# Kernel optimization log

Hardware: AMD Instinct MI355X
Metric: run time of the kernel (lower is better)

## Reference

```python
import jax, jax.numpy as jnp
import numpy as np

B_, T_, DIN, H, DZ, DX = 64, 256, 128, 256, 8, 8


def setup_inputs() -> dict:
    key = jax.random.key(0)
    ks = jax.random.split(key, 13)
    p = lambda k, sh: jax.random.normal(k, sh, dtype=jnp.float32) * 0.05
    return {
        "y": jax.random.normal(ks[0], (B_, T_, DIN), dtype=jnp.float32),
        "W_ih": p(ks[1], (3 * H, DIN)), "W_hh": p(ks[2], (3 * H, H)),
        "b_ih": p(ks[3], (3 * H,)), "b_hh": p(ks[4], (3 * H,)),
        "W_mz": p(ks[5], (DZ, H)), "b_mz": p(ks[6], (DZ,)),
        "W_mx": p(ks[7], (DX, H)), "b_mx": p(ks[8], (DX,)),
        "W_pz": p(ks[9], (2 * DZ, H)), "b_pz": p(ks[10], (2 * DZ,)),
        "W_cx": p(ks[11], (DX * DX, H)), "b_cx": p(ks[12], (DX * DX,)),
    }


def _gru(y, W_ih, W_hh, b_ih, b_hh):
    # torch nn.GRU (single layer, unidirectional, batch_first)
    B, T, _ = y.shape
    Hh = W_hh.shape[1]
    x_proj = jnp.einsum('btd,gd->btg', y, W_ih) + b_ih  # [B,T,3H]

    def step(h, xp):
        hp = h @ W_hh.T + b_hh
        xr, xz, xn = jnp.split(xp, 3, axis=-1)
        hr, hz, hn = jnp.split(hp, 3, axis=-1)
        r = jax.nn.sigmoid(xr + hr)
        z = jax.nn.sigmoid(xz + hz)
        n = jnp.tanh(xn + r * hn)
        h_new = (1.0 - z) * n + z * h
        return h_new, h_new

    h0 = jnp.zeros((B, Hh), dtype=y.dtype)
    _, hs = jax.lax.scan(step, h0, jnp.swapaxes(x_proj, 0, 1))
    return jnp.swapaxes(hs, 0, 1)  # [B,T,H]


def _forward(y, W_ih, W_hh, b_ih, b_hh, W_mz, b_mz, W_mx, b_mx, W_pz, b_pz, W_cx, b_cx):
    enc = _gru(y, W_ih, W_hh, b_ih, b_hh)                       # [B,T,H]
    mean_z = enc @ W_mz.T + b_mz                                 # [B,T,DZ]
    mean_x = enc @ W_mx.T + b_mx                                 # [B,T,DX]
    bd_z = enc @ W_pz.T + b_pz                                   # [B,T,2*DZ]  (apply_softplus=False)

    # banded cov: per latent dim, upper-bidiagonal cholesky factor [B,T,T]
    diag = jnp.moveaxis(jax.nn.softplus(bd_z[..., :DZ]), -1, 0)  # [DZ,B,T]
    off = jnp.moveaxis(bd_z[:, :-1, DZ:], -1, 0)                 # [DZ,B,T-1]
    B, T = diag.shape[1], diag.shape[2]
    idx = jnp.arange(T)
    chol_z = (jnp.zeros((DZ, B, T, T), dtype=y.dtype)
              .at[:, :, idx, idx].set(diag)
              .at[:, :, idx[:-1], idx[1:]].set(off))             # [DZ,B,T,T]

    # anchor first two x-dims at t=0 (in-place mutation in torch)
    mean_x = mean_x.at[:, :, :2].add(-mean_x[:, 0:1, :2])
    mean_x_flat = mean_x.reshape(B * T, DX)

    cov_x = enc @ W_cx.T + b_cx                                  # [B,T,DX*DX]
    cov_x_flat = cov_x.reshape(B * T, DX, DX)
    return mean_z, chol_z, mean_x_flat, cov_x_flat


def reference(y, W_ih, W_hh, b_ih, b_hh, W_mz, b_mz, W_mx, b_mx, W_pz, b_pz, W_cx, b_cx):
    return _forward(y, W_ih, W_hh, b_ih, b_hh, W_mz, b_mz, W_mx, b_mx, W_pz, b_pz, W_cx, b_cx)
```

## Files before the change

kernel.cpp:

```cpp
#include <hip/hip_runtime.h>
#include <cstdint>
#include <cstddef>

#define B_   64
#define T_   256
#define DIN_ 128
#define H_   256
#define G3_  768

__device__ __forceinline__ unsigned short f2h(float f) {
  _Float16 h = (_Float16)f;
  return __builtin_bit_cast(unsigned short, h);
}

__device__ __forceinline__ void dot2f(float& acc, unsigned a, unsigned b) {
  asm("v_dot2_f32_f16 %0, %1, %2, %0" : "+v"(acc) : "v"(a), "v"(b));
}

__global__ __launch_bounds__(256) void prep_kernel(
    const float* __restrict__ W_ih, const float* __restrict__ W_hh,
    const float* __restrict__ W_mz, const float* __restrict__ W_mx,
    const float* __restrict__ W_pz, const float* __restrict__ W_cx,
    float* __restrict__ WT_ih, float* __restrict__ WheadT,
    unsigned* __restrict__ Wreg) {
  int i = blockIdx.x * 256 + threadIdx.x;
  if (i < 98304) {
    int k = i / 768, g = i % 768;
    WT_ih[i] = W_ih[g * 128 + k];
  } else if (i < 98304 + 24576) {
    int j = i - 98304;
    int c = j >> 8, k = j & 255;
    float v;
    if (c < 8)       v = W_mz[c * 256 + k];
    else if (c < 16) v = W_mx[(c - 8) * 256 + k];
    else if (c < 32) v = W_pz[(c - 16) * 256 + k];
    else             v = W_cx[(c - 32) * 256 + k];
    WheadT[j] = v;
  } else {
    int m = i - 122880;
    int c = m & 3, n = m >> 2;
    int t = n & 511, j4 = n >> 9;
    int j = 4 * j4 + c;
    int a = j >> 5, qp = j & 31;
    int o = a * 128 + (t & 127);
    int k0 = ((t >> 7) << 6) + 2 * qp;
    unsigned short lo = f2h(W_hh[o * 256 + k0]);
    unsigned short hi = f2h(W_hh[o * 256 + k0 + 1]);
    Wreg[m] = ((unsigned)hi << 16) | (unsigned)lo;
  }
}

__global__ __launch_bounds__(256) void xproj_kernel(
    const float* __restrict__ y, const float* __restrict__ WT_ih,
    const float* __restrict__ b_ih, float* __restrict__ xp) {
  __shared__ float ylds[32][132];
  int tid = threadIdx.x;
  int row0 = blockIdx.x * 32;
  const float4* y4 = (const float4*)(y + (size_t)row0 * DIN_);
#pragma unroll
  for (int i = 0; i < 4; ++i) {
    int idx = i * 256 + tid;
    float4 v = y4[idx];
    int r = idx >> 5, c4 = (idx & 31) * 4;
    ylds[r][c4 + 0] = v.x; ylds[r][c4 + 1] = v.y;
    ylds[r][c4 + 2] = v.z; ylds[r][c4 + 3] = v.w;
  }
  __syncthreads();
  int tx = tid & 15, ty = tid >> 4;
  for (int c = 0; c < 6; ++c) {
    int col0 = c * 128 + tx * 8;
    float acc[2][8];
#pragma unroll
    for (int a = 0; a < 2; ++a)
#pragma unroll
      for (int b = 0; b < 8; ++b) acc[a][b] = 0.f;
#pragma unroll 4
    for (int k = 0; k < 128; ++k) {
      float4 w0 = *(const float4*)&WT_ih[k * 768 + col0];
      float4 w1 = *(const float4*)&WT_ih[k * 768 + col0 + 4];
      float a0 = ylds[ty * 2 + 0][k], a1 = ylds[ty * 2 + 1][k];
      acc[0][0] += a0 * w0.x; acc[0][1] += a0 * w0.y; acc[0][2] += a0 * w0.z; acc[0][3] += a0 * w0.w;
      acc[0][4] += a0 * w1.x; acc[0][5] += a0 * w1.y; acc[0][6] += a0 * w1.z; acc[0][7] += a0 * w1.w;
      acc[1][0] += a1 * w0.x; acc[1][1] += a1 * w0.y; acc[1][2] += a1 * w0.z; acc[1][3] += a1 * w0.w;
      acc[1][4] += a1 * w1.x; acc[1][5] += a1 * w1.y; acc[1][6] += a1 * w1.z; acc[1][7] += a1 * w1.w;
    }
    float4 b0 = *(const float4*)&b_ih[col0];
    float4 b1 = *(const float4*)&b_ih[col0 + 4];
#pragma unroll
    for (int a = 0; a < 2; ++a) {
      int row = row0 + ty * 2 + a;
      float4 o0, o1;
      o0.x = acc[a][0] + b0.x; o0.y = acc[a][1] + b0.y; o0.z = acc[a][2] + b0.z; o0.w = acc[a][3] + b0.w;
      o1.x = acc[a][4] + b1.x; o1.y = acc[a][5] + b1.y; o1.z = acc[a][6] + b1.z; o1.w = acc[a][7] + b1.w;
      *(float4*)&xp[(size_t)row * G3_ + col0] = o0;
      *(float4*)&xp[(size_t)row * G3_ + col0 + 4] = o1;
    }
  }
}

__global__ __launch_bounds__(512) __attribute__((amdgpu_waves_per_eu(2, 2)))
void gru_kernel(
    const float* __restrict__ xp, const unsigned* Wreg,
    const float* __restrict__ b_hh, float* enc) {
  int tid = threadIdx.x;
  int ks = tid >> 7;
  int og = tid & 127;
  int b = blockIdx.x;
  __shared__ alignas(16) unsigned short hsb[256];
  __shared__ alignas(16) float part[3104];
  unsigned w[192];
  const uint4* W4 = (const uint4*)Wreg;
#pragma unroll
  for (int j4 = 0; j4 < 48; ++j4) {
    uint4 q = W4[j4 * 512 + tid];
    w[4 * j4 + 0] = q.x; w[4 * j4 + 1] = q.y;
    w[4 * j4 + 2] = q.z; w[4 * j4 + 3] = q.w;
  }
  const float* xpb = xp + (size_t)b * (T_ * G3_);
  float* encb = enc + (size_t)b * (T_ * H_);
  float bhr = 0.f, bhz = 0.f, bhn = 0.f, hold = 0.f;
  float xr0 = 0.f, xz0 = 0.f, xn0 = 0.f, xr1 = 0.f, xz1 = 0.f, xn1 = 0.f;
  if (tid < 256) {
    bhr = b_hh[tid]; bhz = b_hh[256 + tid]; bhn = b_hh[512 + tid];
    xr0 = xpb[tid];        xz0 = xpb[256 + tid];        xn0 = xpb[512 + tid];
    xr1 = xpb[768 + tid];  xz1 = xpb[1024 + tid];       xn1 = xpb[1280 + tid];
    hsb[tid] = 0;
  }
  __syncthreads();
  for (int t = 0; t < T_; ++t) {
    asm volatile("" ::: "memory");
    float xr2 = 0.f, xz2 = 0.f, xn2 = 0.f;
    if (tid < 256) {
      int base = (t + 2) * G3_ + tid;
      xr2 = xpb[base]; xz2 = xpb[base + 256]; xn2 = xpb[base + 512];
    }
    float p0 = 0.f, p1 = 0.f, p2 = 0.f, p3 = 0.f, p4 = 0.f, p5 = 0.f;
    const uint4* hs = ((const uint4*)hsb) + (ks << 3);
#pragma unroll
    for (int r = 0; r < 8; ++r) {
      uint4 hq = hs[r];
      dot2f(p0, hq.x, w[(r << 2) + 0]);
      dot2f(p0, hq.y, w[(r << 2) + 1]);
      dot2f(p0, hq.z, w[(r << 2) + 2]);
      dot2f(p0, hq.w, w[(r << 2) + 3]);
      dot2f(p1, hq.x, w[32 + (r << 2) + 0]);
      dot2f(p1, hq.y, w[32 + (r << 2) + 1]);
      dot2f(p1, hq.z, w[32 + (r << 2) + 2]);
      dot2f(p1, hq.w, w[32 + (r << 2) + 3]);
      dot2f(p2, hq.x, w[64 + (r << 2) + 0]);
      dot2f(p2, hq.y, w[64 + (r << 2) + 1]);
      dot2f(p2, hq.z, w[64 + (r << 2) + 2]);
      dot2f(p2, hq.w, w[64 + (r << 2) + 3]);
      dot2f(p3, hq.x, w[96 + (r << 2) + 0]);
      dot2f(p3, hq.y, w[96 + (r << 2) + 1]);
      dot2f(p3, hq.z, w[96 + (r << 2) + 2]);
      dot2f(p3, hq.w, w[96 + (r << 2) + 3]);
      dot2f(p4, hq.x, w[128 + (r << 2) + 0]);
      dot2f(p4, hq.y, w[128 + (r << 2) + 1]);
      dot2f(p4, hq.z, w[128 + (r << 2) + 2]);
      dot2f(p4, hq.w, w[128 + (r << 2) + 3]);
      dot2f(p5, hq.x, w[160 + (r << 2) + 0]);
      dot2f(p5, hq.y, w[160 + (r << 2) + 1]);
      dot2f(p5, hq.z, w[160 + (r << 2) + 2]);
      dot2f(p5, hq.w, w[160 + (r << 2) + 3]);
    }
    int pb = ks * 776 + og;
    part[pb]       = p0;  part[pb + 128] = p1;
    part[pb + 256] = p2;  part[pb + 384] = p3;
    part[pb + 512] = p4;  part[pb + 640] = p5;
    __syncthreads();
    if (tid < 256) {
      int u = tid;
      float prer = bhr + ((part[u] + part[776 + u]) +
                          (part[1552 + u] + part[2328 + u]));
      float prez = bhz + ((part[256 + u] + part[1032 + u]) +
                          (part[1808 + u] + part[2584 + u]));
      float pren = bhn + ((part[512 + u] + part[1288 + u]) +
                          (part[2064 + u] + part[2840 + u]));
      float r_ = 1.f / (1.f + __expf(-(xr0 + prer)));
      float z_ = 1.f / (1.f + __expf(-(xz0 + prez)));
      float a = xn0 + r_ * pren;
      a = fminf(15.f, fmaxf(-15.f, a));
      float e = __expf(2.f * a);
      float n = (e - 1.f) / (e + 1.f);
      float hnew = (1.f - z_) * n + z_ * hold;
      hold = hnew;
      encb[t * H_ + u] = hnew;
      hsb[u] = f2h(hnew);
      xr0 = xr1; xz0 = xz1; xn0 = xn1;
      xr1 = xr2; xz1 = xz2; xn1 = xn2;
    }
    __syncthreads();
  }
}

__global__ void anchor_kernel(const float* __restrict__ enc,
                              const float* __restrict__ W_mx,
                              const float* __restrict__ b_mx,
                              float* __restrict__ anchor) {
  int tid = threadIdx.x;
  if (tid < 128) {
    int b = tid >> 1, d = tid & 1;
    const float* e = enc + (size_t)b * T_ * H_;
    float acc = b_mx[d];
    for (int k = 0; k < 256; ++k) acc += e[k] * W_mx[d * 256 + k];
    anchor[b * 2 + d] = acc;
  }
}

__global__ __launch_bounds__(384) void heads_kernel(
    const float* __restrict__ enc, const float* __restrict__ WheadT,
    const float* __restrict__ b_mz, const float* __restrict__ b_mx,
    const float* __restrict__ b_pz, const float* __restrict__ b_cx,
    const float* __restrict__ anchor,
    float* __restrict__ out_meanz, float* __restrict__ out_meanx,
    float* __restrict__ out_covx, float* __restrict__ stage) {
  __shared__ float el[32 * 256];
  int tid = threadIdx.x;
  int row0 = blockIdx.x * 32;
  const float4* e4 = (const float4*)(enc + (size_t)row0 * 256);
  float4* el4 = (float4*)el;
#pragma unroll
  for (int i = 0; i < 6; ++i) {
    int idx = i * 384 + tid;
    if (idx < 2048) el4[idx] = e4[idx];
  }
  __syncthreads();
  int rg = tid / 96, c = tid - rg * 96;
  const float4* Wc = (const float4*)(WheadT + c * 256);
  float acc[8];
#pragma unroll
  for (int r = 0; r < 8; ++r) acc[r] = 0.f;
  for (int k4 = 0; k4 < 64; ++k4) {
    float4 w4 = Wc[k4];
#pragma unroll
    for (int r = 0; r < 8; ++r) {
      float4 ev = el4[(rg * 8 + r) * 64 + k4];
      acc[r] += w4.x * ev.x; acc[r] += w4.y * ev.y;
      acc[r] += w4.z * ev.z; acc[r] += w4.w * ev.w;
    }
  }
#pragma unroll
  for (int r = 0; r < 8; ++r) {
    int row = row0 + rg * 8 + r;
    int bb = row >> 8;
    float a_ = acc[r];
    if (c < 8) {
      out_meanz[(size_t)row * 8 + c] = a_ + b_mz[c];
    } else if (c < 16) {
      int d = c - 8;
      float v = a_ + b_mx[d];
      if (d < 2) v -= anchor[bb * 2 + d];
      out_meanx[(size_t)row * 8 + d] = v;
    } else if (c < 32) {
      int d = c - 16;
      float v = a_ + b_pz[d];
      if (d < 8)
        v = (v > 0.f) ? (v + log1pf(__expf(-v))) : log1pf(__expf(v));
      stage[(size_t)row * 16 + d] = v;
    } else {
      int d = c - 32;
      out_covx[(size_t)row * 64 + d] = a_ + b_cx[d];
    }
  }
}

__global__ __launch_bounds__(256) void chol_kernel(
    const float* __restrict__ stage, float4* __restrict__ chol) {
  int i = blockIdx.x * 256 + threadIdx.x;
  int stride = gridDim.x * 256;
  for (; i < 8388608; i += stride) {
    int d = i >> 20;
    int bt = (i >> 6) & 16383;
    int t = bt & 255;
    int lane = i & 63;
    float vd = 0.f, vo = 0.f;
    if ((t >> 2) == lane)        vd = stage[bt * 16 + d];
    if (((t + 1) >> 2) == lane)  vo = stage[bt * 16 + 8 + d];
    int te = t & 3, oe = (t + 1) & 3;
    float4 v;
    v.x = (te == 0 ? vd : 0.f) + (oe == 0 ? vo : 0.f);
    v.y = (te == 1 ? vd : 0.f) + (oe == 1 ? vo : 0.f);
    v.z = (te == 2 ? vd : 0.f) + (oe == 2 ? vo : 0.f);
    v.w = (te == 3 ? vd : 0.f) + (oe == 3 ? vo : 0.f);
    chol[i] = v;
  }
}

extern "C" void kernel_launch(void* const* d_in, const int* in_sizes, int n_in,
                              void* d_out, int out_size, void* d_ws, size_t ws_size,
                              hipStream_t stream) {
  const float* y    = (const float*)d_in[0];
  const float* W_ih = (const float*)d_in[1];
  const float* W_hh = (const float*)d_in[2];
  const float* b_ih = (const float*)d_in[3];
  const float* b_hh = (const float*)d_in[4];
  const float* W_mz = (const float*)d_in[5];
  const float* b_mz = (const float*)d_in[6];
  const float* W_mx = (const float*)d_in[7];
  const float* b_mx = (const float*)d_in[8];
  const float* W_pz = (const float*)d_in[9];
  const float* b_pz = (const float*)d_in[10];
  const float* W_cx = (const float*)d_in[11];
  const float* b_cx = (const float*)d_in[12];

  float* out    = (float*)d_out;
  float* mean_z = out;
  float* chol   = out + 131072;
  float* mean_x = out + 33685504;
  float* cov_x  = out + 33816576;

  float* ws      = (float*)d_ws;
  float* WT_ih   = ws;
  float* WheadT  = ws + 98304;
  unsigned* Wreg = (unsigned*)(ws + 122880);
  float* anchor  = ws + 221184;
  float* stage   = ws + 221312;

  float* xp  = chol;
  float* enc = chol + 12582912;

  prep_kernel<<<864, 256, 0, stream>>>(W_ih, W_hh, W_mz, W_mx, W_pz, W_cx,
                                       WT_ih, WheadT, Wreg);
  xproj_kernel<<<512, 256, 0, stream>>>(y, WT_ih, b_ih, xp);
  gru_kernel<<<64, 512, 0, stream>>>(xp, Wreg, b_hh, enc);
  anchor_kernel<<<1, 128, 0, stream>>>(enc, W_mx, b_mx, anchor);
  heads_kernel<<<512, 384, 0, stream>>>(enc, WheadT, b_mz, b_mx, b_pz, b_cx,
                                        anchor, mean_z, mean_x, cov_x, stage);
  chol_kernel<<<8192, 256, 0, stream>>>(stage, (float4*)chol);
}
```

Measured before the change: 620.3 us.

## Fuse input projection into GRU kernel with flag-based streaming and split chol zeroing

Merges the x-projection GEMM and the GRU recurrence into one launch. 64 recurrence blocks spin on per-chunk release/acquire flags while 256 extra blocks compute xp in 64-row chunks, so the recurrence can start before the whole projection finishes. It also parallelises the anchor reduction across 128 blocks. The zero-fill of the upper half of chol_z (latent dims 4-7) moves into extra heads_kernel blocks, and chol_fin only writes the diagonals for those dims, which shortens the tail pass. The cost is a forward-progress dependency: the spin-waiting blocks need the producer blocks to be scheduled alongside them, plus extra flag traffic.

```diff
diff --git a/kernel.cpp b/kernel.cpp
--- a/kernel.cpp
+++ b/kernel.cpp
@@ -17,13 +17,18 @@
   asm("v_dot2_f32_f16 %0, %1, %2, %0" : "+v"(acc) : "v"(a), "v"(b));
 }
 
+__device__ __forceinline__ int load_acq(const int* p) {
+  return __hip_atomic_load(p, __ATOMIC_ACQUIRE, __HIP_MEMORY_SCOPE_AGENT);
+}
+
 __global__ __launch_bounds__(256) void prep_kernel(
     const float* __restrict__ W_ih, const float* __restrict__ W_hh,
     const float* __restrict__ W_mz, const float* __restrict__ W_mx,
     const float* __restrict__ W_pz, const float* __restrict__ W_cx,
     float* __restrict__ WT_ih, float* __restrict__ WheadT,
-    unsigned* __restrict__ Wreg) {
+    unsigned* __restrict__ Wreg, int* __restrict__ done) {
   int i = blockIdx.x * 256 + threadIdx.x;
+  if (i < 512) done[i] = 0;
   if (i < 98304) {
     int k = i / 768, g = i % 768;
     WT_ih[i] = W_ih[g * 128 + k];
@@ -50,64 +55,73 @@
   }
 }
 
-__global__ __launch_bounds__(256) void xproj_kernel(
+__global__ __launch_bounds__(512) __attribute__((amdgpu_waves_per_eu(2, 2)))
+void fused_kernel(
     const float* __restrict__ y, const float* __restrict__ WT_ih,
-    const float* __restrict__ b_ih, float* __restrict__ xp) {
-  __shared__ float ylds[32][132];
+    const float* __restrict__ b_ih, float* xp,
+    const unsigned* Wreg, const float* __restrict__ b_hh,
+    float* enc, int* done) {
+  __shared__ alignas(16) unsigned char smem[34816];
   int tid = threadIdx.x;
-  int row0 = blockIdx.x * 32;
-  const float4* y4 = (const float4*)(y + (size_t)row0 * DIN_);
-#pragma unroll
-  for (int i = 0; i < 4; ++i) {
-    int idx = i * 256 + tid;
-    float4 v = y4[idx];
-    int r = idx >> 5, c4 = (idx & 31) * 4;
-    ylds[r][c4 + 0] = v.x; ylds[r][c4 + 1] = v.y;
-    ylds[r][c4 + 2] = v.z; ylds[r][c4 + 3] = v.w;
-  }
-  __syncthreads();
-  int tx = tid & 15, ty = tid >> 4;
-  for (int c = 0; c < 6; ++c) {
-    int col0 = c * 128 + tx * 8;
-    float acc[2][8];
-#pragma unroll
-    for (int a = 0; a < 2; ++a)
-#pragma unroll
-      for (int b = 0; b < 8; ++b) acc[a][b] = 0.f;
+
+  if (blockIdx.x >= 64) {
+    int j = blockIdx.x - 64;
+    int row0 = j * 64;
+    float* ylds = (float*)smem;
+    const float4* y4 = (const float4*)(y + (size_t)row0 * DIN_);
+#pragma unroll
+    for (int i = 0; i < 4; ++i) {
+      int idx = i * 512 + tid;
+      float4 v = y4[idx];
+      int r = idx >> 5, c4 = (idx & 31) * 4;
+      ylds[r * 132 + c4 + 0] = v.x; ylds[r * 132 + c4 + 1] = v.y;
+      ylds[r * 132 + c4 + 2] = v.z; ylds[r * 132 + c4 + 3] = v.w;
+    }
+    __syncthreads();
+    int tx = tid & 15, ty = tid >> 4;
+    for (int c = 0; c < 6; ++c) {
+      int col0 = c * 128 + tx * 8;
+      float acc[2][8];
+#pragma unroll
+      for (int a = 0; a < 2; ++a)
+#pragma unroll
+        for (int b2 = 0; b2 < 8; ++b2) acc[a][b2] = 0.f;
 #pragma unroll 4
-    for (int k = 0; k < 128; ++k) {
-      float4 w0 = *(const float4*)&WT_ih[k * 768 + col0];
-      float4 w1 = *(const float4*)&WT_ih[k * 768 + col0 + 4];
-      float a0 = ylds[ty * 2 + 0][k], a1 = ylds[ty * 2 + 1][k];
-      acc[0][0] += a0 * w0.x; acc[0][1] += a0 * w0.y; acc[0][2] += a0 * w0.z; acc[0][3] += a0 * w0.w;
-      acc[0][4] += a0 * w1.x; acc[0][5] += a0 * w1.y; acc[0][6] += a0 * w1.z; acc[0][7] += a0 * w1.w;
-      acc[1][0] += a1 * w0.x; acc[1][1] += a1 * w0.y; acc[1][2] += a1 * w0.z; acc[1][3] += a1 * w0.w;
-      acc[1][4] += a1 * w1.x; acc[1][5] += a1 * w1.y; acc[1][6] += a1 * w1.z; acc[1][7] += a1 * w1.w;
-    }
-    float4 b0 = *(const float4*)&b_ih[col0];
-    float4 b1 = *(const float4*)&b_ih[col0 + 4];
-#pragma unroll
-    for (int a = 0; a < 2; ++a) {
-      int row = row0 + ty * 2 + a;
-      float4 o0, o1;
-      o0.x = acc[a][0] + b0.x; o0.y = acc[a][1] + b0.y; o0.z = acc[a][2] + b0.z; o0.w = acc[a][3] + b0.w;
-      o1.x = acc[a][4] + b1.x; o1.y = acc[a][5] + b1.y; o1.z = acc[a][6] + b1.z; o1.w = acc[a][7] + b1.w;
-      *(float4*)&xp[(size_t)row * G3_ + col0] = o0;
-      *(float4*)&xp[(size_t)row * G3_ + col0 + 4] = o1;
-    }
-  }
-}
-
-__global__ __launch_bounds__(512) __attribute__((amdgpu_waves_per_eu(2, 2)))
-void gru_kernel(
-    const float* __restrict__ xp, const unsigned* Wreg,
-    const float* __restrict__ b_hh, float* enc) {
-  int tid = threadIdx.x;
+      for (int k = 0; k < 128; ++k) {
+        float4 w0 = *(const float4*)&WT_ih[k * 768 + col0];
+        float4 w1 = *(const float4*)&WT_ih[k * 768 + col0 + 4];
+        float a0 = ylds[(ty * 2 + 0) * 132 + k];
+        float a1 = ylds[(ty * 2 + 1) * 132 + k];
+        acc[0][0] += a0 * w0.x; acc[0][1] += a0 * w0.y; acc[0][2] += a0 * w0.z; acc[0][3] += a0 * w0.w;
+        acc[0][4] += a0 * w1.x; acc[0][5] += a0 * w1.y; acc[0][6] += a0 * w1.z; acc[0][7] += a0 * w1.w;
+        acc[1][0] += a1 * w0.x; acc[1][1] += a1 * w0.y; acc[1][2] += a1 * w0.z; acc[1][3] += a1 * w0.w;
+        acc[1][4] += a1 * w1.x; acc[1][5] += a1 * w1.y; acc[1][6] += a1 * w1.z; acc[1][7] += a1 * w1.w;
+      }
+      float4 b0 = *(const float4*)&b_ih[col0];
+      float4 b1 = *(const float4*)&b_ih[col0 + 4];
+#pragma unroll
+      for (int a = 0; a < 2; ++a) {
+        int row = row0 + ty * 2 + a;
+        float4 o0, o1;
+        o0.x = acc[a][0] + b0.x; o0.y = acc[a][1] + b0.y; o0.z = acc[a][2] + b0.z; o0.w = acc[a][3] + b0.w;
+        o1.x = acc[a][4] + b1.x; o1.y = acc[a][5] + b1.y; o1.z = acc[a][6] + b1.z; o1.w = acc[a][7] + b1.w;
+        *(float4*)&xp[(size_t)row * G3_ + col0] = o0;
+        *(float4*)&xp[(size_t)row * G3_ + col0 + 4] = o1;
+      }
+    }
+    __syncthreads();
+    if (tid == 0) {
+      __threadfence();
+      __hip_atomic_store(&done[j], 1, __ATOMIC_RELEASE, __HIP_MEMORY_SCOPE_AGENT);
+    }
+    return;
+  }
+
   int ks = tid >> 7;
   int og = tid & 127;
   int b = blockIdx.x;
-  __shared__ alignas(16) unsigned short hsb[256];
-  __shared__ alignas(16) float part[3104];
+  unsigned short* hsb = (unsigned short*)smem;
+  float* part = (float*)(smem + 512);
   unsigned w[192];
   const uint4* W4 = (const uint4*)Wreg;
 #pragma unroll
@@ -118,6 +132,8 @@
   }
   const float* xpb = xp + (size_t)b * (T_ * G3_);
   float* encb = enc + (size_t)b * (T_ * H_);
+  if (tid == 0) { while (load_acq(&done[4 * b]) == 0) {} }
+  __syncthreads();
   float bhr = 0.f, bhz = 0.f, bhn = 0.f, hold = 0.f;
   float xr0 = 0.f, xz0 = 0.f, xn0 = 0.f, xr1 = 0.f, xz1 = 0.f, xn1 = 0.f;
   if (tid < 256) {
@@ -128,9 +144,16 @@
   }
   __syncthreads();
   for (int t = 0; t < T_; ++t) {
+    if (t == 62 || t == 126 || t == 190) {
+      if (tid == 0) {
+        const int* f = &done[4 * b + ((t + 2) >> 6)];
+        while (load_acq(f) == 0) {}
+      }
+      __syncthreads();
+    }
     asm volatile("" ::: "memory");
     float xr2 = 0.f, xz2 = 0.f, xn2 = 0.f;
-    if (tid < 256) {
+    if (tid < 256 && t < 254) {
       int base = (t + 2) * G3_ + tid;
       xr2 = xpb[base]; xz2 = xpb[base + 256]; xn2 = xpb[base + 512];
     }
@@ -194,18 +217,19 @@
   }
 }
 
-__global__ void anchor_kernel(const float* __restrict__ enc,
-                              const float* __restrict__ W_mx,
-                              const float* __restrict__ b_mx,
-                              float* __restrict__ anchor) {
-  int tid = threadIdx.x;
-  if (tid < 128) {
-    int b = tid >> 1, d = tid & 1;
-    const float* e = enc + (size_t)b * T_ * H_;
-    float acc = b_mx[d];
-    for (int k = 0; k < 256; ++k) acc += e[k] * W_mx[d * 256 + k];
-    anchor[b * 2 + d] = acc;
-  }
+__global__ __launch_bounds__(256) void anchor_kernel(
+    const float* __restrict__ enc, const float* __restrict__ W_mx,
+    const float* __restrict__ b_mx, float* __restrict__ anchor) {
+  __shared__ float red[4];
+  int bid = blockIdx.x, tid = threadIdx.x;
+  int b = bid >> 1, d = bid & 1;
+  float v = enc[(size_t)b * (T_ * H_) + tid] * W_mx[d * 256 + tid];
+#pragma unroll
+  for (int off = 32; off >= 1; off >>= 1) v += __shfl_down(v, off, 64);
+  if ((tid & 63) == 0) red[tid >> 6] = v;
+  __syncthreads();
+  if (tid == 0)
+    anchor[b * 2 + d] = b_mx[d] + ((red[0] + red[1]) + (red[2] + red[3]));
 }
 
 __global__ __launch_bounds__(384) void heads_kernel(
@@ -214,7 +238,15 @@
     const float* __restrict__ b_pz, const float* __restrict__ b_cx,
     const float* __restrict__ anchor,
     float* __restrict__ out_meanz, float* __restrict__ out_meanx,
-    float* __restrict__ out_covx, float* __restrict__ stage) {
+    float* __restrict__ out_covx, float* __restrict__ stage,
+    float4* __restrict__ chol4) {
+  if (blockIdx.x >= 512) {
+    float4* cz = chol4 + 4194304;
+    int idx = (blockIdx.x - 512) * 384 + threadIdx.x;
+    float4 z = {0.f, 0.f, 0.f, 0.f};
+    for (; idx < 4194304; idx += 192 * 384) cz[idx] = z;
+    return;
+  }
   __shared__ float el[32 * 256];
   int tid = threadIdx.x;
   int row0 = blockIdx.x * 32;
@@ -265,25 +297,38 @@
   }
 }
 
-__global__ __launch_bounds__(256) void chol_kernel(
+__global__ __launch_bounds__(256) void chol_fin(
     const float* __restrict__ stage, float4* __restrict__ chol) {
   int i = blockIdx.x * 256 + threadIdx.x;
   int stride = gridDim.x * 256;
-  for (; i < 8388608; i += stride) {
-    int d = i >> 20;
-    int bt = (i >> 6) & 16383;
-    int t = bt & 255;
-    int lane = i & 63;
-    float vd = 0.f, vo = 0.f;
-    if ((t >> 2) == lane)        vd = stage[bt * 16 + d];
-    if (((t + 1) >> 2) == lane)  vo = stage[bt * 16 + 8 + d];
-    int te = t & 3, oe = (t + 1) & 3;
-    float4 v;
-    v.x = (te == 0 ? vd : 0.f) + (oe == 0 ? vo : 0.f);
-    v.y = (te == 1 ? vd : 0.f) + (oe == 1 ? vo : 0.f);
-    v.z = (te == 2 ? vd : 0.f) + (oe == 2 ? vo : 0.f);
-    v.w = (te == 3 ? vd : 0.f) + (oe == 3 ? vo : 0.f);
-    chol[i] = v;
+  for (; i < 4325376; i += stride) {
+    if (i < 4194304) {
+      int d = i >> 20;
+      int bt = (i >> 6) & 16383;
+      int t = bt & 255;
+      int lane = i & 63;
+      float vd = 0.f, vo = 0.f;
+      if ((t >> 2) == lane)       vd = stage[bt * 16 + d];
+      if (((t + 1) >> 2) == lane) vo = stage[bt * 16 + 8 + d];
+      int te = t & 3, oe = (t + 1) & 3;
+      float4 v;
+      v.x = (te == 0 ? vd : 0.f) + (oe == 0 ? vo : 0.f);
+      v.y = (te == 1 ? vd : 0.f) + (oe == 1 ? vo : 0.f);
+      v.z = (te == 2 ? vd : 0.f) + (oe == 2 ? vo : 0.f);
+      v.w = (te == 3 ? vd : 0.f) + (oe == 3 ? vo : 0.f);
+      chol[i] = v;
+    } else {
+      int j = i - 4194304;
+      int bt = j >> 3, q = j & 7;
+      int bb = bt >> 8, tt = bt & 255;
+      int d = 4 + (q & 3);
+      float* ch = (float*)chol;
+      if (q < 4) {
+        ch[(((size_t)d * 64 + bb) * 256 + tt) * 256 + tt] = stage[bt * 16 + d];
+      } else if (tt < 255) {
+        ch[(((size_t)d * 64 + bb) * 256 + tt) * 256 + tt + 1] = stage[bt * 16 + 8 + d];
+      }
+    }
   }
 }
 
@@ -316,16 +361,18 @@
   unsigned* Wreg = (unsigned*)(ws + 122880);
   float* anchor  = ws + 221184;
   float* stage   = ws + 221312;
+  int*   done    = (int*)(ws + 483456);
 
   float* xp  = chol;
   float* enc = chol + 12582912;
 
   prep_kernel<<<864, 256, 0, stream>>>(W_ih, W_hh, W_mz, W_mx, W_pz, W_cx,
-                                       WT_ih, WheadT, Wreg);
-  xproj_kernel<<<512, 256, 0, stream>>>(y, WT_ih, b_ih, xp);
-  gru_kernel<<<64, 512, 0, stream>>>(xp, Wreg, b_hh, enc);
-  anchor_kernel<<<1, 128, 0, stream>>>(enc, W_mx, b_mx, anchor);
-  heads_kernel<<<512, 384, 0, stream>>>(enc, WheadT, b_mz, b_mx, b_pz, b_cx,
-                                        anchor, mean_z, mean_x, cov_x, stage);
-  chol_kernel<<<8192, 256, 0, stream>>>(stage, (float4*)chol);
-}
+                                       WT_ih, WheadT, Wreg, done);
+  fused_kernel<<<320, 512, 0, stream>>>(y, WT_ih, b_ih, xp, Wreg, b_hh,
+                                        enc, done);
+  anchor_kernel<<<128, 256, 0, stream>>>(enc, W_mx, b_mx, anchor);
+  heads_kernel<<<704, 384, 0, stream>>>(enc, WheadT, b_mz, b_mx, b_pz, b_cx,
+                                        anchor, mean_z, mean_x, cov_x, stage,
+                                        (float4*)chol);
+  chol_fin<<<4096, 256, 0, stream>>>(stage, (float4*)chol);
+}
```

Measured after the change: 774.4 us. 1.25x slower.

## Fuse anchor and chol zero-fill into heads kernel, enlarge xproj tile

Applied to the files above, without the earlier changes.

Removes the single-block anchor kernel by computing anchors in extra blocks of the heads kernel using wave reductions, and uses other extra blocks to zero-fill the upper half of the chol output, which does not overlap enc. The chol kernel then writes the lower half fully plus scattered diagonal and off-diagonal entries for the upper half, and subtracts the anchor from mean_x afterward. The xproj tile is doubled to 64 rows per block for more register reuse of the weights. This cuts launches and overlaps the zero-fill with head computation, at the cost of more registers in xproj and scattered writes.

```diff
diff --git a/kernel.cpp b/kernel.cpp
--- a/kernel.cpp
+++ b/kernel.cpp
@@ -53,12 +53,12 @@
 __global__ __launch_bounds__(256) void xproj_kernel(
     const float* __restrict__ y, const float* __restrict__ WT_ih,
     const float* __restrict__ b_ih, float* __restrict__ xp) {
-  __shared__ float ylds[32][132];
+  __shared__ float ylds[64][132];
   int tid = threadIdx.x;
-  int row0 = blockIdx.x * 32;
+  int row0 = blockIdx.x * 64;
   const float4* y4 = (const float4*)(y + (size_t)row0 * DIN_);
 #pragma unroll
-  for (int i = 0; i < 4; ++i) {
+  for (int i = 0; i < 8; ++i) {
     int idx = i * 256 + tid;
     float4 v = y4[idx];
     int r = idx >> 5, c4 = (idx & 31) * 4;
@@ -69,26 +69,31 @@
   int tx = tid & 15, ty = tid >> 4;
   for (int c = 0; c < 6; ++c) {
     int col0 = c * 128 + tx * 8;
-    float acc[2][8];
-#pragma unroll
-    for (int a = 0; a < 2; ++a)
+    float acc[4][8];
+#pragma unroll
+    for (int a = 0; a < 4; ++a)
 #pragma unroll
       for (int b = 0; b < 8; ++b) acc[a][b] = 0.f;
 #pragma unroll 4
     for (int k = 0; k < 128; ++k) {
       float4 w0 = *(const float4*)&WT_ih[k * 768 + col0];
       float4 w1 = *(const float4*)&WT_ih[k * 768 + col0 + 4];
-      float a0 = ylds[ty * 2 + 0][k], a1 = ylds[ty * 2 + 1][k];
+      float a0 = ylds[ty * 4 + 0][k], a1 = ylds[ty * 4 + 1][k];
+      float a2 = ylds[ty * 4 + 2][k], a3 = ylds[ty * 4 + 3][k];
       acc[0][0] += a0 * w0.x; acc[0][1] += a0 * w0.y; acc[0][2] += a0 * w0.z; acc[0][3] += a0 * w0.w;
       acc[0][4] += a0 * w1.x; acc[0][5] += a0 * w1.y; acc[0][6] += a0 * w1.z; acc[0][7] += a0 * w1.w;
       acc[1][0] += a1 * w0.x; acc[1][1] += a1 * w0.y; acc[1][2] += a1 * w0.z; acc[1][3] += a1 * w0.w;
       acc[1][4] += a1 * w1.x; acc[1][5] += a1 * w1.y; acc[1][6] += a1 * w1.z; acc[1][7] += a1 * w1.w;
+      acc[2][0] += a2 * w0.x; acc[2][1] += a2 * w0.y; acc[2][2] += a2 * w0.z; acc[2][3] += a2 * w0.w;
+      acc[2][4] += a2 * w1.x; acc[2][5] += a2 * w1.y; acc[2][6] += a2 * w1.z; acc[2][7] += a2 * w1.w;
+      acc[3][0] += a3 * w0.x; acc[3][1] += a3 * w0.y; acc[3][2] += a3 * w0.z; acc[3][3] += a3 * w0.w;
+      acc[3][4] += a3 * w1.x; acc[3][5] += a3 * w1.y; acc[3][6] += a3 * w1.z; acc[3][7] += a3 * w1.w;
     }
     float4 b0 = *(const float4*)&b_ih[col0];
     float4 b1 = *(const float4*)&b_ih[col0 + 4];
 #pragma unroll
-    for (int a = 0; a < 2; ++a) {
-      int row = row0 + ty * 2 + a;
+    for (int a = 0; a < 4; ++a) {
+      int row = row0 + ty * 4 + a;
       float4 o0, o1;
       o0.x = acc[a][0] + b0.x; o0.y = acc[a][1] + b0.y; o0.z = acc[a][2] + b0.z; o0.w = acc[a][3] + b0.w;
       o1.x = acc[a][4] + b1.x; o1.y = acc[a][5] + b1.y; o1.z = acc[a][6] + b1.z; o1.w = acc[a][7] + b1.w;
@@ -194,29 +199,38 @@
   }
 }
 
-__global__ void anchor_kernel(const float* __restrict__ enc,
-                              const float* __restrict__ W_mx,
-                              const float* __restrict__ b_mx,
-                              float* __restrict__ anchor) {
-  int tid = threadIdx.x;
-  if (tid < 128) {
-    int b = tid >> 1, d = tid & 1;
-    const float* e = enc + (size_t)b * T_ * H_;
-    float acc = b_mx[d];
-    for (int k = 0; k < 256; ++k) acc += e[k] * W_mx[d * 256 + k];
-    anchor[b * 2 + d] = acc;
-  }
-}
-
 __global__ __launch_bounds__(384) void heads_kernel(
     const float* __restrict__ enc, const float* __restrict__ WheadT,
     const float* __restrict__ b_mz, const float* __restrict__ b_mx,
     const float* __restrict__ b_pz, const float* __restrict__ b_cx,
-    const float* __restrict__ anchor,
     float* __restrict__ out_meanz, float* __restrict__ out_meanx,
-    float* __restrict__ out_covx, float* __restrict__ stage) {
+    float* __restrict__ out_covx, float* __restrict__ stage,
+    float4* __restrict__ chol4, float* __restrict__ anchor,
+    const float* __restrict__ W_mx) {
+  int tid = threadIdx.x;
+  if (blockIdx.x >= 704) {
+    __shared__ float red[4];
+    int bid = blockIdx.x - 704;
+    int b = bid >> 1, d = bid & 1;
+    if (tid < 256) {
+      float v = enc[(size_t)b * (T_ * H_) + tid] * W_mx[d * 256 + tid];
+#pragma unroll
+      for (int off = 32; off >= 1; off >>= 1) v += __shfl_down(v, off, 64);
+      if ((tid & 63) == 0) red[tid >> 6] = v;
+    }
+    __syncthreads();
+    if (tid == 0)
+      anchor[b * 2 + d] = b_mx[d] + ((red[0] + red[1]) + (red[2] + red[3]));
+    return;
+  }
+  if (blockIdx.x >= 512) {
+    float4* cz = chol4 + 4194304;
+    int idx = (blockIdx.x - 512) * 384 + tid;
+    float4 z = {0.f, 0.f, 0.f, 0.f};
+    for (; idx < 4194304; idx += 192 * 384) cz[idx] = z;
+    return;
+  }
   __shared__ float el[32 * 256];
-  int tid = threadIdx.x;
   int row0 = blockIdx.x * 32;
   const float4* e4 = (const float4*)(enc + (size_t)row0 * 256);
   float4* el4 = (float4*)el;
@@ -243,15 +257,12 @@
 #pragma unroll
   for (int r = 0; r < 8; ++r) {
     int row = row0 + rg * 8 + r;
-    int bb = row >> 8;
     float a_ = acc[r];
     if (c < 8) {
       out_meanz[(size_t)row * 8 + c] = a_ + b_mz[c];
     } else if (c < 16) {
       int d = c - 8;
-      float v = a_ + b_mx[d];
-      if (d < 2) v -= anchor[bb * 2 + d];
-      out_meanx[(size_t)row * 8 + d] = v;
+      out_meanx[(size_t)row * 8 + d] = a_ + b_mx[d];
     } else if (c < 32) {
       int d = c - 16;
       float v = a_ + b_pz[d];
@@ -265,25 +276,43 @@
   }
 }
 
-__global__ __launch_bounds__(256) void chol_kernel(
-    const float* __restrict__ stage, float4* __restrict__ chol) {
+__global__ __launch_bounds__(256) void chol_fin(
+    const float* __restrict__ stage, float4* __restrict__ chol,
+    const float* __restrict__ anchor, float* __restrict__ mean_x) {
   int i = blockIdx.x * 256 + threadIdx.x;
   int stride = gridDim.x * 256;
-  for (; i < 8388608; i += stride) {
-    int d = i >> 20;
-    int bt = (i >> 6) & 16383;
-    int t = bt & 255;
-    int lane = i & 63;
-    float vd = 0.f, vo = 0.f;
-    if ((t >> 2) == lane)        vd = stage[bt * 16 + d];
-    if (((t + 1) >> 2) == lane)  vo = stage[bt * 16 + 8 + d];
-    int te = t & 3, oe = (t + 1) & 3;
-    float4 v;
-    v.x = (te == 0 ? vd : 0.f) + (oe == 0 ? vo : 0.f);
-    v.y = (te == 1 ? vd : 0.f) + (oe == 1 ? vo : 0.f);
-    v.z = (te == 2 ? vd : 0.f) + (oe == 2 ? vo : 0.f);
-    v.w = (te == 3 ? vd : 0.f) + (oe == 3 ? vo : 0.f);
-    chol[i] = v;
+  for (; i < 4358144; i += stride) {
+    if (i < 4194304) {
+      int d = i >> 20;
+      int bt = (i >> 6) & 16383;
+      int t = bt & 255;
+      int lane = i & 63;
+      float vd = 0.f, vo = 0.f;
+      if ((t >> 2) == lane)       vd = stage[bt * 16 + d];
+      if (((t + 1) >> 2) == lane) vo = stage[bt * 16 + 8 + d];
+      int te = t & 3, oe = (t + 1) & 3;
+      float4 v;
+      v.x = (te == 0 ? vd : 0.f) + (oe == 0 ? vo : 0.f);
+      v.y = (te == 1 ? vd : 0.f) + (oe == 1 ? vo : 0.f);
+      v.z = (te == 2 ? vd : 0.f) + (oe == 2 ? vo : 0.f);
+      v.w = (te == 3 ? vd : 0.f) + (oe == 3 ? vo : 0.f);
+      chol[i] = v;
+    } else if (i < 4325376) {
+      int j = i - 4194304;
+      int bt = j >> 3, q = j & 7;
+      int bb = bt >> 8, tt = bt & 255;
+      int d = 4 + (q & 3);
+      float* ch = (float*)chol;
+      if (q < 4) {
+        ch[(((size_t)d * 64 + bb) * 256 + tt) * 256 + tt] = stage[bt * 16 + d];
+      } else if (tt < 255) {
+        ch[(((size_t)d * 64 + bb) * 256 + tt) * 256 + tt + 1] = stage[bt * 16 + 8 + d];
+      }
+    } else {
+      int j2 = i - 4325376;
+      int row = j2 >> 1, d = j2 & 1;
+      mean_x[(size_t)row * 8 + d] -= anchor[(row >> 8) * 2 + d];
+    }
   }
 }
 
@@ -322,10 +351,10 @@
 
   prep_kernel<<<864, 256, 0, stream>>>(W_ih, W_hh, W_mz, W_mx, W_pz, W_cx,
                                        WT_ih, WheadT, Wreg);
-  xproj_kernel<<<512, 256, 0, stream>>>(y, WT_ih, b_ih, xp);
+  xproj_kernel<<<256, 256, 0, stream>>>(y, WT_ih, b_ih, xp);
   gru_kernel<<<64, 512, 0, stream>>>(xp, Wreg, b_hh, enc);
-  anchor_kernel<<<1, 128, 0, stream>>>(enc, W_mx, b_mx, anchor);
-  heads_kernel<<<512, 384, 0, stream>>>(enc, WheadT, b_mz, b_mx, b_pz, b_cx,
-                                        anchor, mean_z, mean_x, cov_x, stage);
-  chol_kernel<<<8192, 256, 0, stream>>>(stage, (float4*)chol);
-}
+  heads_kernel<<<832, 384, 0, stream>>>(enc, WheadT, b_mz, b_mx, b_pz, b_cx,
+                                        mean_z, mean_x, cov_x, stage,
+                                        (float4*)chol, anchor, W_mx);
+  chol_fin<<<4096, 256, 0, stream>>>(stage, (float4*)chol, anchor, mean_x);
+}
```

New measurement: 599.7 us. 3.3% less time.
